# Kernel tuning notes

Measured on AMD Instinct MI355X. Metric: run time of the kernel, lower is better.

The kernel has to match this reference:

```python
import jax, jax.numpy as jnp
import numpy as np

N_NODES = 100000
N_EDGES = 1600000
NFEAT = 128
NHID = 128
NS = 64
NCLASS = 16
B = 8192


def setup_inputs() -> dict:
    key = jax.random.key(0)
    ks = jax.random.split(key, 12)
    s = jax.random.normal(ks[0], (B, NS), dtype=jnp.float32)
    x = jax.random.normal(ks[1], (N_NODES, NFEAT), dtype=jnp.float32)
    row = jax.random.randint(ks[2], (N_EDGES,), 0, N_NODES)
    col = jax.random.randint(ks[3], (N_EDGES,), 0, N_NODES)
    val = jax.random.uniform(ks[4], (N_EDGES,), dtype=jnp.float32)
    index = jax.random.randint(ks[5], (B,), 0, N_NODES)
    # learned parameters (glorot-ish scale)
    W1 = jax.random.normal(ks[6], (NFEAT, NHID), dtype=jnp.float32) / np.sqrt(NFEAT)
    b1 = jnp.zeros((NHID,), dtype=jnp.float32)
    W2 = jax.random.normal(ks[7], (NHID, NHID), dtype=jnp.float32) / np.sqrt(NHID)
    b2 = jnp.zeros((NHID,), dtype=jnp.float32)
    Wl = jax.random.normal(ks[8], (NHID + NS, NCLASS), dtype=jnp.float32) / np.sqrt(NHID + NS)
    bl = jnp.zeros((NCLASS,), dtype=jnp.float32)
    return {"s": s, "x": x, "row": row, "col": col, "val": val,
            "index": index, "W1": W1, "b1": b1, "W2": W2, "b2": b2,
            "Wl": Wl, "bl": bl}


def reference(s, x, row, col, val, index, W1, b1, W2, b2, Wl, bl):
    n = x.shape[0]

    def spmm(h):
        # adj @ h with adj in COO form: out[r] += val_e * h[c]
        return jax.ops.segment_sum(val[:, None] * h[col], row, num_segments=n)

    # dropout is identity in eval mode (training=False)
    h = jax.nn.relu(spmm(x @ W1) + b1)          # gc1 + relu
    h = spmm(h @ W2) + b2                        # gc2
    z = jnp.concatenate([h[index], s], axis=1) @ Wl + bl  # [B, nclass]
    return jax.nn.log_softmax(z, axis=1)
```

## Files before the change

kernel.cpp:

```cpp
#include <hip/hip_runtime.h>
#include <hip/hip_fp16.h>
#include <math.h>

#define N_NODES 100000
#define N_EDGES 1600000
#define NFEAT 128
#define NHID 128
#define NS 64
#define NCLASS 16
#define BB 8192

#define B1_SHIFT 11
#define NB1 49
#define SUB_SHIFT 5
#define NSUB 3125
#define CHUNKA 2048
#define HWG 256
#define BINC_CAP 2048

#define NSLICE 8
#define SLICEF 16

typedef unsigned long long ull;
typedef unsigned int uint;


__device__ __forceinline__ unsigned short f2bf(float f) {
  unsigned int u = __float_as_uint(f);
  return (unsigned short)((u + 0x7fffu + ((u >> 16) & 1u)) >> 16);
}
__device__ __forceinline__ unsigned int packbf2(float lo, float hi) {
  return (unsigned int)f2bf(lo) | ((unsigned int)f2bf(hi) << 16);
}


__device__ __forceinline__ __half2 h2zero() {
  return __builtin_bit_cast(__half2, 0u);
}
__device__ __forceinline__ __half2 h2shfl_add(__half2 a, int m) {
  int t = __shfl_xor(__builtin_bit_cast(int, a), m);
  return __hadd2(a, __builtin_bit_cast(__half2, t));
}
__device__ __forceinline__ uint relu2(uint u) {
  uint mm = ((u >> 15) & 0x10001u) * 0xFFFFu;
  return u & ~mm;
}
union U4H { uint4 u4; __half2 h[4]; };

__device__ __forceinline__ void fma_row_h(__half2* acc, __half2 v, uint4 u) {
  U4H q; q.u4 = u;
#pragma unroll
  for (int k = 0; k < 4; ++k) acc[k] = __hfma2(v, q.h[k], acc[k]);
}
__device__ __forceinline__ __half2 edge_vh2(uint e) {
  uint hb = e >> 17;
  return __builtin_bit_cast(__half2, hb * 0x10001u);
}


__device__ __forceinline__ ull pack_edge(float v, int r, int c) {
  return ((ull)(__float_as_uint(v) >> 2) << 34) | ((ull)(unsigned)r << 17) | (unsigned)c;
}
__device__ __forceinline__ int edge_col(ull p) { return (int)(p & 0x1FFFFu); }
__device__ __forceinline__ int edge_row(ull p) { return (int)((unsigned)(p >> 17) & 0x1FFFFu); }
__device__ __forceinline__ float edge_val(ull p) {
  return __uint_as_float(((unsigned)(p >> 34)) << 2);
}
__device__ __forceinline__ uint pack4(ull p) {
  uint hb = (uint)__half_as_ushort(__float2half(edge_val(p)));
  return (uint)edge_col(p) | (hb << 17);
}
__device__ __forceinline__ int keep_test(const uint* keep, int r) {
  return (keep[r >> 5] >> (r & 31)) & 1u;
}


__global__ __launch_bounds__(256) void selbuild_kernel(const int* __restrict__ index,
                                                       int* __restrict__ sel,
                                                       uint* __restrict__ keep) {
  int t = blockIdx.x * 256 + threadIdx.x;
  int r = index[t];
  sel[r] = 1;
  atomicOr(&keep[r >> 5], 1u << (r & 31));
}

__global__ __launch_bounds__(256) void selflag_kernel(const int* __restrict__ row,
                                                      const int* __restrict__ col,
                                                      const int* __restrict__ sel,
                                                      uint* __restrict__ keep) {
  int i = blockIdx.x * blockDim.x + threadIdx.x;
  int stride = gridDim.x * blockDim.x;
  for (; i < N_EDGES; i += stride)
    if (sel[row[i]]) {
      int c = col[i];
      atomicOr(&keep[c >> 5], 1u << (c & 31));
    }
}


__global__ __launch_bounds__(256) void rdesc_kernel(const uint* __restrict__ keep,
                                                    const int* __restrict__ offs,
                                                    ull* __restrict__ rdesc,
                                                    int* __restrict__ nkept) {
  int w = blockIdx.x * 256 + threadIdx.x;
  if (w >= NSUB) return;
  uint b = keep[w];
  int c = __popc(b);
  if (!c) return;
  int base = atomicAdd(nkept, c);
  int r0 = w << 5;
  while (b) {
    int i = __ffs(b) - 1;
    int r = r0 + i;
    int s0 = offs[r], s1 = offs[r + 1];
    rdesc[base++] = (ull)(uint)r | ((ull)(uint)s0 << 17) | ((ull)(uint)(s1 - s0) << 39);
    b &= b - 1;
  }
}

__global__ __launch_bounds__(256) void sdesc_kernel(const int* __restrict__ index,
                                                    const int* __restrict__ offs,
                                                    ull* __restrict__ sdesc) {
  int b = blockIdx.x * 256 + threadIdx.x;
  int r = index[b];
  int s0 = offs[r];
  sdesc[b] = (ull)(uint)s0 | ((ull)(uint)(offs[r + 1] - s0) << 22);
}


__global__ __launch_bounds__(256) void histsub_kernel(const int* __restrict__ row,
                                                      const uint* __restrict__ keep,
                                                      int* __restrict__ subcnt) {
  __shared__ int lh[NSUB];
  int tid = threadIdx.x;
  for (int i = tid; i < NSUB; i += 256) lh[i] = 0;
  __syncthreads();
  for (long i = (long)blockIdx.x * 256 + tid; i < N_EDGES; i += (long)HWG * 256) {
    int r = row[i];
    if (keep_test(keep, r)) atomicAdd(&lh[r >> SUB_SHIFT], 1);
  }
  __syncthreads();
  for (int i = tid; i < NSUB; i += 256) {
    int c = lh[i];
    if (c) atomicAdd(&subcnt[i], c);
  }
}


__global__ __launch_bounds__(1024) void scanall_kernel(const int* __restrict__ subcnt,
                                                       int* __restrict__ sub_offs,
                                                       int* __restrict__ gcur1,
                                                       int* __restrict__ gcur2) {
  __shared__ int sd[1024];
  int tid = threadIdx.x;
  int b0 = tid * 4;
  int vv[4];
  int loc = 0;
#pragma unroll
  for (int k = 0; k < 4; ++k) {
    int i = b0 + k;
    vv[k] = (i < NSUB) ? subcnt[i] : 0;
    loc += vv[k];
  }
  sd[tid] = loc;
  __syncthreads();
  for (int o = 1; o < 1024; o <<= 1) {
    int add = (tid >= o) ? sd[tid - o] : 0;
    __syncthreads();
    sd[tid] += add;
    __syncthreads();
  }
  int pre = sd[tid] - loc;
#pragma unroll
  for (int k = 0; k < 4; ++k) {
    int i = b0 + k;
    if (i < NSUB) {
      sub_offs[i] = pre;
      gcur2[i] = pre;
      if ((i & 63) == 0) gcur1[i >> 6] = pre;
      pre += vv[k];
    }
  }
  if (tid == 1023) sub_offs[NSUB] = sd[1023];
}


__global__ __launch_bounds__(256) void binA_kernel(const int* __restrict__ row,
                                                   const int* __restrict__ col,
                                                   const float* __restrict__ val,
                                                   const uint* __restrict__ keep,
                                                   int* __restrict__ gcur1,
                                                   ull* __restrict__ ebuf1) {
  __shared__ ull stage[CHUNKA];
  __shared__ short bkt[CHUNKA];
  __shared__ int hist[NB1], lofs[NB1 + 1], lcur[NB1], gbase[NB1];
  int tid = threadIdx.x;
  for (long base = (long)blockIdx.x * CHUNKA; base < N_EDGES; base += (long)gridDim.x * CHUNKA) {
    int cnt = (int)min((long)CHUNKA, (long)N_EDGES - base);
    if (tid < NB1) hist[tid] = 0;
    __syncthreads();
    ull e[8]; int bk[8];
#pragma unroll
    for (int v = 0; v < 8; ++v) {
      int i = v * 256 + tid;
      bk[v] = -1;
      if (i < cnt) {
        long g = base + i;
        int r = row[g];
        if (keep_test(keep, r)) {
          e[v] = pack_edge(val[g], r, col[g]);
          bk[v] = r >> B1_SHIFT;
          atomicAdd(&hist[bk[v]], 1);
        }
      }
    }
    __syncthreads();
    if (tid < 64) {
      int h = (tid < NB1) ? hist[tid] : 0;
      int x = h;
      for (int o = 1; o < 64; o <<= 1) {
        int y = __shfl_up(x, o);
        if (tid >= o) x += y;
      }
      if (tid < NB1) { lofs[tid] = x - h; lcur[tid] = x - h; }
      if (tid == 63) lofs[NB1] = x;
    }
    __syncthreads();
#pragma unroll
    for (int v = 0; v < 8; ++v) {
      if (bk[v] >= 0) {
        int pos = atomicAdd(&lcur[bk[v]], 1);
        stage[pos] = e[v];
        bkt[pos] = (short)bk[v];
      }
    }
    __syncthreads();
    if (tid < NB1) {
      int h = hist[tid];
      if (h > 0) gbase[tid] = atomicAdd(&gcur1[tid], h);
    }
    __syncthreads();
    int tot = lofs[NB1];
    for (int s = tid; s < tot; s += 256) {
      int lo = bkt[s];
      ebuf1[gbase[lo] + (s - lofs[lo])] = stage[s];
    }
    __syncthreads();
  }
}


__global__ __launch_bounds__(256) void binB_kernel(const ull* __restrict__ ebuf1,
                                                   const int* __restrict__ sub_offs,
                                                   int* __restrict__ gcur2,
                                                   ull* __restrict__ edat8) {
  __shared__ ull stage[CHUNKA];
  __shared__ short bkt[CHUNKA];
  __shared__ int hist[64], lofs[65], lcur[64], gbase[64];
  int tid = threadIdx.x;
  int b1 = blockIdx.x >> 3, w = blockIdx.x & 7;
  int rbeg = sub_offs[b1 << 6];
  int rend = sub_offs[min((b1 + 1) << 6, NSUB)];
  for (int base = rbeg + w * CHUNKA; base < rend; base += 8 * CHUNKA) {
    int cnt = min(CHUNKA, rend - base);
    if (tid < 64) hist[tid] = 0;
    __syncthreads();
    ull e[8]; int bk[8];
#pragma unroll
    for (int v = 0; v < 8; ++v) {
      int i = v * 256 + tid;
      bk[v] = -1;
      if (i < cnt) {
        e[v] = ebuf1[base + i];
        bk[v] = (edge_row(e[v]) >> SUB_SHIFT) - (b1 << 6);
        atomicAdd(&hist[bk[v]], 1);
      }
    }
    __syncthreads();
    if (tid < 64) {
      int h = hist[tid];
      int x = h;
      for (int o = 1; o < 64; o <<= 1) {
        int y = __shfl_up(x, o);
        if (tid >= o) x += y;
      }
      lofs[tid] = x - h;
      lcur[tid] = x - h;
      if (tid == 63) lofs[64] = x;
    }
    __syncthreads();
#pragma unroll
    for (int v = 0; v < 8; ++v) {
      if (bk[v] >= 0) {
        int pos = atomicAdd(&lcur[bk[v]], 1);
        stage[pos] = e[v];
        bkt[pos] = (short)bk[v];
      }
    }
    __syncthreads();
    if (tid < 64) {
      int h = hist[tid];
      if (h > 0) gbase[tid] = atomicAdd(&gcur2[(b1 << 6) + tid], h);
    }
    __syncthreads();
    for (int s = tid; s < cnt; s += 256) {
      int lo = bkt[s];
      edat8[gbase[lo] + (s - lofs[lo])] = stage[s];
    }
    __syncthreads();
  }
}


__global__ __launch_bounds__(256) void binC_kernel(const int* __restrict__ sub_offs,
                                                   const ull* __restrict__ edat8,
                                                   ull* __restrict__ ebuf1,
                                                   uint* __restrict__ edat4,
                                                   int* __restrict__ offs) {
  __shared__ ull es[BINC_CAP];
  __shared__ int rcnt[32], rcur[32];
  int s = blockIdx.x, tid = threadIdx.x;
  int r0 = s << SUB_SHIFT;
  int beg = sub_offs[s], end = sub_offs[s + 1];
  int n = end - beg;
  if (tid < 32) rcnt[tid] = 0;
  __syncthreads();
  if (n <= BINC_CAP) {
    for (int i = tid; i < n; i += 256) {
      ull p = edat8[beg + i];
      es[i] = p;
      atomicAdd(&rcnt[edge_row(p) & 31], 1);
    }
    __syncthreads();
    if (tid < 32) {
      int h = rcnt[tid];
      int x = h;
      for (int o = 1; o < 32; o <<= 1) {
        int y = __shfl_up(x, o, 32);
        if (tid >= o) x += y;
      }
      rcur[tid] = x - h;
      offs[r0 + tid] = beg + x - h;
      if (s == NSUB - 1 && tid == 31) offs[N_NODES] = end;
    }
    __syncthreads();
    for (int i = tid; i < n; i += 256) {
      ull p = es[i];
      int pos = atomicAdd(&rcur[edge_row(p) & 31], 1);
      edat4[beg + pos] = pack4(p);
    }
  } else {
    for (int i = tid; i < n; i += 256) {
      ull p = edat8[beg + i];
      ebuf1[beg + i] = p;
      atomicAdd(&rcnt[edge_row(p) & 31], 1);
    }
    __syncthreads();
    if (tid < 32) {
      int h = rcnt[tid];
      int x = h;
      for (int o = 1; o < 32; o <<= 1) {
        int y = __shfl_up(x, o, 32);
        if (tid >= o) x += y;
      }
      rcur[tid] = x - h;
      offs[r0 + tid] = beg + x - h;
      if (s == NSUB - 1 && tid == 31) offs[N_NODES] = end;
    }
    __syncthreads();
    for (int i = tid; i < n; i += 256) {
      ull p = ebuf1[beg + i];
      int pos = atomicAdd(&rcur[edge_row(p) & 31], 1);
      edat4[beg + pos] = pack4(p);
    }
  }
}


typedef __attribute__((ext_vector_type(8))) __bf16 bf16x8;
typedef __attribute__((ext_vector_type(4))) float f32x4;
union FragU { uint4 u; bf16x8 b; };

#define LDSTR 68

__global__ __launch_bounds__(256) void gemm1_kernel(const float* __restrict__ A,
                                                    const float* __restrict__ W,
                                                    unsigned short* __restrict__ C,
                                                    int nrows) {
  __shared__ uint As_s[64 * LDSTR];
  __shared__ uint Wt_s[128 * LDSTR];
  int tid = threadIdx.x;
  int rbase = blockIdx.x * 64;

  {
    int n = tid & 127, hh = tid >> 7;
#pragma unroll
    for (int kk = 0; kk < 32; ++kk) {
      int kc = hh * 32 + kk;
      Wt_s[n * LDSTR + kc] = packbf2(W[(2 * kc) * 128 + n], W[(2 * kc + 1) * 128 + n]);
    }
  }
  {
    const float4* src = (const float4*)(A + (long)rbase * 128);
#pragma unroll
    for (int i = 0; i < 8; ++i) {
      int f = i * 256 + tid;
      int m = f >> 5;
      float4 v = (rbase + m < nrows) ? src[f] : make_float4(0.f, 0.f, 0.f, 0.f);
      int c = (f & 31) * 2;
      As_s[m * LDSTR + c]     = packbf2(v.x, v.y);
      As_s[m * LDSTR + c + 1] = packbf2(v.z, v.w);
    }
  }
  __syncthreads();

  int w = tid >> 6, lane = tid & 63;
  int quad = lane >> 4, lr = lane & 15;
  int n0 = w * 32;

  f32x4 acc[4][2];
#pragma unroll
  for (int mt = 0; mt < 4; ++mt)
#pragma unroll
    for (int nt = 0; nt < 2; ++nt) acc[mt][nt] = (f32x4){0.f, 0.f, 0.f, 0.f};

#pragma unroll
  for (int kk = 0; kk < 4; ++kk) {
    int kc = kk * 16 + quad * 4;
    FragU fb0, fb1;
    fb0.u = *(const uint4*)&Wt_s[(n0 + lr) * LDSTR + kc];
    fb1.u = *(const uint4*)&Wt_s[(n0 + 16 + lr) * LDSTR + kc];
#pragma unroll
    for (int mt = 0; mt < 4; ++mt) {
      FragU fa;
      fa.u = *(const uint4*)&As_s[(mt * 16 + lr) * LDSTR + kc];
      acc[mt][0] = __builtin_amdgcn_mfma_f32_16x16x32_bf16(fa.b, fb0.b, acc[mt][0], 0, 0, 0);
      acc[mt][1] = __builtin_amdgcn_mfma_f32_16x16x32_bf16(fa.b, fb1.b, acc[mt][1], 0, 0, 0);
    }
  }

#pragma unroll
  for (int mt = 0; mt < 4; ++mt) {
#pragma unroll
    for (int nt = 0; nt < 2; ++nt) {
      __half* cs = (__half*)(C + (size_t)(w * 2 + nt) * (N_NODES * SLICEF));
#pragma unroll
      for (int r = 0; r < 4; ++r) {
        int row = rbase + mt * 16 + quad * 4 + r;
        if (row < nrows) cs[(size_t)row * SLICEF + lr] = __float2half(acc[mt][nt][r]);
      }
    }
  }
}


__global__ __launch_bounds__(256) void gemm2f_kernel(const float* __restrict__ g2,
                                                     const float* __restrict__ W2,
                                                     const float* __restrict__ b2,
                                                     const float* __restrict__ s_in,
                                                     const float* __restrict__ Wl,
                                                     const float* __restrict__ bl,
                                                     float* __restrict__ out) {
  __shared__ uint smem[13056];
  uint* Wt_s = smem;
  uint* As_s = smem + 128 * LDSTR;
  float* ts  = (float*)smem;
  float* Wls = (float*)(smem + 128 * LDSTR);
  int tid = threadIdx.x;
  int rbase = blockIdx.x * 64;

  {
    int n = tid & 127, hh = tid >> 7;
#pragma unroll
    for (int kk = 0; kk < 32; ++kk) {
      int kc = hh * 32 + kk;
      Wt_s[n * LDSTR + kc] = packbf2(W2[(2 * kc) * 128 + n], W2[(2 * kc + 1) * 128 + n]);
    }
  }
  {
    const float4* src = (const float4*)(g2 + (long)rbase * 128);
#pragma unroll
    for (int i = 0; i < 8; ++i) {
      int f = i * 256 + tid;
      int m = f >> 5, c = (f & 31) * 2;
      float4 v = src[f];
      As_s[m * LDSTR + c]     = packbf2(v.x, v.y);
      As_s[m * LDSTR + c + 1] = packbf2(v.z, v.w);
    }
  }
  __syncthreads();

  int w = tid >> 6, lane = tid & 63;
  int quad = lane >> 4, lr = lane & 15;
  int n0 = w * 32;

  f32x4 acc[4][2];
#pragma unroll
  for (int mt = 0; mt < 4; ++mt)
#pragma unroll
    for (int nt = 0; nt < 2; ++nt) acc[mt][nt] = (f32x4){0.f, 0.f, 0.f, 0.f};

#pragma unroll
  for (int kk = 0; kk < 4; ++kk) {
    int kc = kk * 16 + quad * 4;
    FragU fb0, fb1;
    fb0.u = *(const uint4*)&Wt_s[(n0 + lr) * LDSTR + kc];
    fb1.u = *(const uint4*)&Wt_s[(n0 + 16 + lr) * LDSTR + kc];
#pragma unroll
    for (int mt = 0; mt < 4; ++mt) {
      FragU fa;
      fa.u = *(const uint4*)&As_s[(mt * 16 + lr) * LDSTR + kc];
      acc[mt][0] = __builtin_amdgcn_mfma_f32_16x16x32_bf16(fa.b, fb0.b, acc[mt][0], 0, 0, 0);
      acc[mt][1] = __builtin_amdgcn_mfma_f32_16x16x32_bf16(fa.b, fb1.b, acc[mt][1], 0, 0, 0);
    }
  }
  __syncthreads();

#pragma unroll
  for (int mt = 0; mt < 4; ++mt) {
#pragma unroll
    for (int nt = 0; nt < 2; ++nt) {
      int col = n0 + nt * 16 + lr;
      float bv = b2[col];
#pragma unroll
      for (int r = 0; r < 4; ++r)
        ts[(mt * 16 + quad * 4 + r) * 129 + col] = acc[mt][nt][r] + bv;
    }
  }
  for (int i = tid; i < 192 * 16; i += 256) Wls[i] = Wl[i];
  __syncthreads();

  int q = lane & 3;
  int mrow = w * 16 + (lane >> 2);
  int b = rbase + mrow;
  float z[16];
#pragma unroll
  for (int c = 0; c < 16; ++c) z[c] = 0.f;
  int k0 = q * 48;
  for (int kk = 0; kk < 48; ++kk) {
    int k = k0 + kk;
    float xv = (k < 128) ? ts[mrow * 129 + k] : s_in[(long)b * 64 + (k - 128)];
    const float* wp = Wls + k * 16;
#pragma unroll
    for (int c = 0; c < 16; ++c) z[c] = fmaf(xv, wp[c], z[c]);
  }
#pragma unroll
  for (int c = 0; c < 16; ++c) {
    z[c] += __shfl_xor(z[c], 1);
    z[c] += __shfl_xor(z[c], 2);
  }
  if (q == 0) {
#pragma unroll
    for (int c = 0; c < 16; ++c) z[c] += bl[c];
    float mx = z[0];
#pragma unroll
    for (int c = 1; c < 16; ++c) mx = fmaxf(mx, z[c]);
    float sum = 0.f;
#pragma unroll
    for (int c = 0; c < 16; ++c) sum += expf(z[c] - mx);
    float lse = mx + logf(sum);
    float4* ob = (float4*)(out + (long)b * 16);
    ob[0] = make_float4(z[0] - lse, z[1] - lse, z[2] - lse, z[3] - lse);
    ob[1] = make_float4(z[4] - lse, z[5] - lse, z[6] - lse, z[7] - lse);
    ob[2] = make_float4(z[8] - lse, z[9] - lse, z[10] - lse, z[11] - lse);
    ob[3] = make_float4(z[12] - lse, z[13] - lse, z[14] - lse, z[15] - lse);
  }
}


__global__ __launch_bounds__(256) void spmm_row_kernel(const ull* __restrict__ rdesc,
                                                       const uint* __restrict__ edat4,
                                                       const unsigned short* __restrict__ a,
                                                       const float* __restrict__ bias,
                                                       unsigned short* __restrict__ h1,
                                                       const int* __restrict__ nkept) {
  int nk = *nkept;
  int rblk = blockIdx.x >> 3;
  if (rblk * 32 >= nk) return;
  int s = blockIdx.x & 7;
  int tid = threadIdx.x, lane = tid & 63;
  int li = rblk * 32 + (tid >> 3);
  int g = (lane >> 1) & 3, h = lane & 1, h8 = h * 8;
  const unsigned short* as = a + (size_t)s * (N_NODES * SLICEF);
  bool active = li < nk;
  int r = 0, j = 0, jend = 0;
  if (active) {
    ull d = rdesc[li];
    r = (int)(d & 0x1FFFFu);
    int start = (int)((d >> 17) & 0x3FFFFFu);
    j = start + g;
    jend = start + (int)(d >> 39);
  }
  __half2 acc[4] = {h2zero(), h2zero(), h2zero(), h2zero()};
  for (; j + 12 < jend; j += 16) {
    uint e0 = edat4[j];
    uint e1 = edat4[j + 4];
    uint e2 = edat4[j + 8];
    uint e3 = edat4[j + 12];
    uint4 u0 = *(const uint4*)(as + (size_t)(e0 & 0x1FFFFu) * SLICEF + h8);
    uint4 u1 = *(const uint4*)(as + (size_t)(e1 & 0x1FFFFu) * SLICEF + h8);
    uint4 u2 = *(const uint4*)(as + (size_t)(e2 & 0x1FFFFu) * SLICEF + h8);
    uint4 u3 = *(const uint4*)(as + (size_t)(e3 & 0x1FFFFu) * SLICEF + h8);
    fma_row_h(acc, edge_vh2(e0), u0);
    fma_row_h(acc, edge_vh2(e1), u1);
    fma_row_h(acc, edge_vh2(e2), u2);
    fma_row_h(acc, edge_vh2(e3), u3);
  }
  if (j + 4 < jend) {
    uint e0 = edat4[j];
    uint e1 = edat4[j + 4];
    uint4 u0 = *(const uint4*)(as + (size_t)(e0 & 0x1FFFFu) * SLICEF + h8);
    uint4 u1 = *(const uint4*)(as + (size_t)(e1 & 0x1FFFFu) * SLICEF + h8);
    fma_row_h(acc, edge_vh2(e0), u0);
    fma_row_h(acc, edge_vh2(e1), u1);
    j += 8;
  }
  if (j < jend) {
    uint e = edat4[j];
    uint4 u = *(const uint4*)(as + (size_t)(e & 0x1FFFFu) * SLICEF + h8);
    fma_row_h(acc, edge_vh2(e), u);
  }
#pragma unroll
  for (int k = 0; k < 4; ++k) {
    acc[k] = h2shfl_add(acc[k], 2);
    acc[k] = h2shfl_add(acc[k], 4);
  }
  if (active && (lane & 6) == 0) {
    const float* bp = bias + s * SLICEF + h8;
    float4 b0 = *(const float4*)bp;
    float4 b1v = *(const float4*)(bp + 4);
    uint4 o;
    o.x = relu2(__builtin_bit_cast(uint, __hadd2(acc[0], __floats2half2_rn(b0.x, b0.y))));
    o.y = relu2(__builtin_bit_cast(uint, __hadd2(acc[1], __floats2half2_rn(b0.z, b0.w))));
    o.z = relu2(__builtin_bit_cast(uint, __hadd2(acc[2], __floats2half2_rn(b1v.x, b1v.y))));
    o.w = relu2(__builtin_bit_cast(uint, __hadd2(acc[3], __floats2half2_rn(b1v.z, b1v.w))));
    *(uint4*)(h1 + (size_t)s * (N_NODES * SLICEF) + (size_t)r * SLICEF + h8) = o;
  }
}

__global__ __launch_bounds__(256) void spmm_sel_kernel(const ull* __restrict__ sdesc,
                                                       const uint* __restrict__ edat4,
                                                       const unsigned short* __restrict__ h1,
                                                       float* __restrict__ g2) {
  int s = blockIdx.x & 7;
  int bblk = blockIdx.x >> 3;
  int tid = threadIdx.x, lane = tid & 63;
  int b = bblk * 32 + (tid >> 3);
  int g = (lane >> 1) & 3, h = lane & 1, h8 = h * 8;
  const unsigned short* hs = h1 + (size_t)s * (N_NODES * SLICEF);
  ull d = sdesc[b];
  int start = (int)(d & 0x3FFFFFu);
  int j = start + g, jend = start + (int)(d >> 22);
  __half2 acc[4] = {h2zero(), h2zero(), h2zero(), h2zero()};
  for (; j + 12 < jend; j += 16) {
    uint e0 = edat4[j];
    uint e1 = edat4[j + 4];
    uint e2 = edat4[j + 8];
    uint e3 = edat4[j + 12];
    uint4 u0 = *(const uint4*)(hs + (size_t)(e0 & 0x1FFFFu) * SLICEF + h8);
    uint4 u1 = *(const uint4*)(hs + (size_t)(e1 & 0x1FFFFu) * SLICEF + h8);
    uint4 u2 = *(const uint4*)(hs + (size_t)(e2 & 0x1FFFFu) * SLICEF + h8);
    uint4 u3 = *(const uint4*)(hs + (size_t)(e3 & 0x1FFFFu) * SLICEF + h8);
    fma_row_h(acc, edge_vh2(e0), u0);
    fma_row_h(acc, edge_vh2(e1), u1);
    fma_row_h(acc, edge_vh2(e2), u2);
    fma_row_h(acc, edge_vh2(e3), u3);
  }
  if (j + 4 < jend) {
    uint e0 = edat4[j];
    uint e1 = edat4[j + 4];
    uint4 u0 = *(const uint4*)(hs + (size_t)(e0 & 0x1FFFFu) * SLICEF + h8);
    uint4 u1 = *(const uint4*)(hs + (size_t)(e1 & 0x1FFFFu) * SLICEF + h8);
    fma_row_h(acc, edge_vh2(e0), u0);
    fma_row_h(acc, edge_vh2(e1), u1);
    j += 8;
  }
  if (j < jend) {
    uint e = edat4[j];
    uint4 u = *(const uint4*)(hs + (size_t)(e & 0x1FFFFu) * SLICEF + h8);
    fma_row_h(acc, edge_vh2(e), u);
  }
#pragma unroll
  for (int k = 0; k < 4; ++k) {
    acc[k] = h2shfl_add(acc[k], 2);
    acc[k] = h2shfl_add(acc[k], 4);
  }
  if ((lane & 6) == 0) {
    float* op = g2 + (size_t)b * 128 + s * SLICEF + h8;
    *(float4*)op = make_float4(__low2float(acc[0]), __high2float(acc[0]),
                               __low2float(acc[1]), __high2float(acc[1]));
    *(float4*)(op + 4) = make_float4(__low2float(acc[2]), __high2float(acc[2]),
                                     __low2float(acc[3]), __high2float(acc[3]));
  }
}


extern "C" void kernel_launch(void* const* d_in, const int* in_sizes, int n_in,
                              void* d_out, int out_size, void* d_ws, size_t ws_size,
                              hipStream_t stream) {
  const float* s_in  = (const float*)d_in[0];
  const float* x     = (const float*)d_in[1];
  const int*   row   = (const int*)d_in[2];
  const int*   col   = (const int*)d_in[3];
  const float* val   = (const float*)d_in[4];
  const int*   index = (const int*)d_in[5];
  const float* W1    = (const float*)d_in[6];
  const float* b1    = (const float*)d_in[7];
  const float* W2    = (const float*)d_in[8];
  const float* b2    = (const float*)d_in[9];
  const float* Wl    = (const float*)d_in[10];
  const float* bl    = (const float*)d_in[11];
  float* out = (float*)d_out;

  ull* edat8 = (ull*)d_ws;
  ull* ebuf1 = edat8 + N_EDGES;
  uint* edat4 = (uint*)ebuf1;
  ull* rdesc = edat8;
  ull* sdesc = edat8 + N_NODES;
  unsigned short* a  = (unsigned short*)(ebuf1 + N_EDGES);
  unsigned short* h1 = a + (size_t)N_NODES * 128;
  float* g2   = (float*)(h1 + (size_t)N_NODES * 128);
  int* sel    = (int*)(g2 + (size_t)BB * 128);
  int* subcnt = sel + N_NODES;
  uint* keep  = (uint*)(subcnt + NSUB);
  int* offs   = (int*)(keep + NSUB);
  int* sub_offs = offs + (N_NODES + 1);
  int* gcur1  = sub_offs + (NSUB + 1);
  int* gcur2  = gcur1 + NB1;
  int* nkept  = gcur2 + NSUB;

  hipMemsetAsync(sel, 0, (N_NODES + 2 * NSUB) * sizeof(int), stream);
  hipMemsetAsync(nkept, 0, sizeof(int), stream);

  selbuild_kernel<<<BB / 256, 256, 0, stream>>>(index, sel, keep);
  selflag_kernel<<<4096, 256, 0, stream>>>(row, col, sel, keep);
  histsub_kernel<<<HWG, 256, 0, stream>>>(row, keep, subcnt);
  scanall_kernel<<<1, 1024, 0, stream>>>(subcnt, sub_offs, gcur1, gcur2);

  binA_kernel<<<512, 256, 0, stream>>>(row, col, val, keep, gcur1, ebuf1);
  binB_kernel<<<NB1 * 8, 256, 0, stream>>>(ebuf1, sub_offs, gcur2, edat8);
  binC_kernel<<<NSUB, 256, 0, stream>>>(sub_offs, edat8, ebuf1, edat4, offs);

  rdesc_kernel<<<(NSUB + 255) / 256, 256, 0, stream>>>(keep, offs, rdesc, nkept);
  sdesc_kernel<<<BB / 256, 256, 0, stream>>>(index, offs, sdesc);

  gemm1_kernel<<<(N_NODES + 63) / 64, 256, 0, stream>>>(x, W1, a, N_NODES);
  spmm_row_kernel<<<NSUB * NSLICE, 256, 0, stream>>>(rdesc, edat4, a, b1, h1, nkept);
  spmm_sel_kernel<<<(BB / 32) * NSLICE, 256, 0, stream>>>(sdesc, edat4, h1, g2);
  gemm2f_kernel<<<BB / 64, 256, 0, stream>>>(g2, W2, b2, s_in, Wl, bl, out);
}
```

Baseline: 317.9 us.

## Replace two-pass LDS-staged binning with direct global-atomic scatter; double gemm1 rows per block

The two-level bucket sort (binA into 49 coarse bins, then binB into 3125 sub-bins) becomes a single kernel in which each kept edge takes its slot with a global atomicAdd on its sub-bucket cursor and writes straight to edat8. This removes one full pass over the edge buffer and the LDS staging, at the cost of heavy global atomic contention and uncoalesced scattered writes. Separately, gemm1 now handles two 64-row tiles per block, so the W1 transpose/convert into LDS is amortised across twice the rows with half as many blocks.

```diff
diff --git a/kernel.cpp b/kernel.cpp
--- a/kernel.cpp
+++ b/kernel.cpp
@@ -10,11 +10,8 @@
 #define NCLASS 16
 #define BB 8192
 
-#define B1_SHIFT 11
-#define NB1 49
 #define SUB_SHIFT 5
 #define NSUB 3125
-#define CHUNKA 2048
 #define HWG 256
 #define BINC_CAP 2048
 
@@ -149,7 +146,6 @@
 
 __global__ __launch_bounds__(1024) void scanall_kernel(const int* __restrict__ subcnt,
                                                        int* __restrict__ sub_offs,
-                                                       int* __restrict__ gcur1,
                                                        int* __restrict__ gcur2) {
   __shared__ int sd[1024];
   int tid = threadIdx.x;
@@ -177,7 +173,6 @@
     if (i < NSUB) {
       sub_offs[i] = pre;
       gcur2[i] = pre;
-      if ((i & 63) == 0) gcur1[i >> 6] = pre;
       pre += vv[k];
     }
   }
@@ -185,129 +180,20 @@
 }
 
 
-__global__ __launch_bounds__(256) void binA_kernel(const int* __restrict__ row,
-                                                   const int* __restrict__ col,
-                                                   const float* __restrict__ val,
-                                                   const uint* __restrict__ keep,
-                                                   int* __restrict__ gcur1,
-                                                   ull* __restrict__ ebuf1) {
-  __shared__ ull stage[CHUNKA];
-  __shared__ short bkt[CHUNKA];
-  __shared__ int hist[NB1], lofs[NB1 + 1], lcur[NB1], gbase[NB1];
-  int tid = threadIdx.x;
-  for (long base = (long)blockIdx.x * CHUNKA; base < N_EDGES; base += (long)gridDim.x * CHUNKA) {
-    int cnt = (int)min((long)CHUNKA, (long)N_EDGES - base);
-    if (tid < NB1) hist[tid] = 0;
-    __syncthreads();
-    ull e[8]; int bk[8];
-#pragma unroll
-    for (int v = 0; v < 8; ++v) {
-      int i = v * 256 + tid;
-      bk[v] = -1;
-      if (i < cnt) {
-        long g = base + i;
-        int r = row[g];
-        if (keep_test(keep, r)) {
-          e[v] = pack_edge(val[g], r, col[g]);
-          bk[v] = r >> B1_SHIFT;
-          atomicAdd(&hist[bk[v]], 1);
-        }
-      }
-    }
-    __syncthreads();
-    if (tid < 64) {
-      int h = (tid < NB1) ? hist[tid] : 0;
-      int x = h;
-      for (int o = 1; o < 64; o <<= 1) {
-        int y = __shfl_up(x, o);
-        if (tid >= o) x += y;
-      }
-      if (tid < NB1) { lofs[tid] = x - h; lcur[tid] = x - h; }
-      if (tid == 63) lofs[NB1] = x;
-    }
-    __syncthreads();
-#pragma unroll
-    for (int v = 0; v < 8; ++v) {
-      if (bk[v] >= 0) {
-        int pos = atomicAdd(&lcur[bk[v]], 1);
-        stage[pos] = e[v];
-        bkt[pos] = (short)bk[v];
-      }
-    }
-    __syncthreads();
-    if (tid < NB1) {
-      int h = hist[tid];
-      if (h > 0) gbase[tid] = atomicAdd(&gcur1[tid], h);
-    }
-    __syncthreads();
-    int tot = lofs[NB1];
-    for (int s = tid; s < tot; s += 256) {
-      int lo = bkt[s];
-      ebuf1[gbase[lo] + (s - lofs[lo])] = stage[s];
-    }
-    __syncthreads();
-  }
-}
-
-
-__global__ __launch_bounds__(256) void binB_kernel(const ull* __restrict__ ebuf1,
-                                                   const int* __restrict__ sub_offs,
-                                                   int* __restrict__ gcur2,
-                                                   ull* __restrict__ edat8) {
-  __shared__ ull stage[CHUNKA];
-  __shared__ short bkt[CHUNKA];
-  __shared__ int hist[64], lofs[65], lcur[64], gbase[64];
-  int tid = threadIdx.x;
-  int b1 = blockIdx.x >> 3, w = blockIdx.x & 7;
-  int rbeg = sub_offs[b1 << 6];
-  int rend = sub_offs[min((b1 + 1) << 6, NSUB)];
-  for (int base = rbeg + w * CHUNKA; base < rend; base += 8 * CHUNKA) {
-    int cnt = min(CHUNKA, rend - base);
-    if (tid < 64) hist[tid] = 0;
-    __syncthreads();
-    ull e[8]; int bk[8];
-#pragma unroll
-    for (int v = 0; v < 8; ++v) {
-      int i = v * 256 + tid;
-      bk[v] = -1;
-      if (i < cnt) {
-        e[v] = ebuf1[base + i];
-        bk[v] = (edge_row(e[v]) >> SUB_SHIFT) - (b1 << 6);
-        atomicAdd(&hist[bk[v]], 1);
-      }
-    }
-    __syncthreads();
-    if (tid < 64) {
-      int h = hist[tid];
-      int x = h;
-      for (int o = 1; o < 64; o <<= 1) {
-        int y = __shfl_up(x, o);
-        if (tid >= o) x += y;
-      }
-      lofs[tid] = x - h;
-      lcur[tid] = x - h;
-      if (tid == 63) lofs[64] = x;
-    }
-    __syncthreads();
-#pragma unroll
-    for (int v = 0; v < 8; ++v) {
-      if (bk[v] >= 0) {
-        int pos = atomicAdd(&lcur[bk[v]], 1);
-        stage[pos] = e[v];
-        bkt[pos] = (short)bk[v];
-      }
-    }
-    __syncthreads();
-    if (tid < 64) {
-      int h = hist[tid];
-      if (h > 0) gbase[tid] = atomicAdd(&gcur2[(b1 << 6) + tid], h);
-    }
-    __syncthreads();
-    for (int s = tid; s < cnt; s += 256) {
-      int lo = bkt[s];
-      edat8[gbase[lo] + (s - lofs[lo])] = stage[s];
-    }
-    __syncthreads();
+__global__ __launch_bounds__(256) void binAB_kernel(const int* __restrict__ row,
+                                                    const int* __restrict__ col,
+                                                    const float* __restrict__ val,
+                                                    const uint* __restrict__ keep,
+                                                    int* __restrict__ gcur2,
+                                                    ull* __restrict__ edat8) {
+  long i = (long)blockIdx.x * 256 + threadIdx.x;
+  long stride = (long)gridDim.x * 256;
+  for (; i < N_EDGES; i += stride) {
+    int r = row[i];
+    if (keep_test(keep, r)) {
+      int pos = atomicAdd(&gcur2[r >> SUB_SHIFT], 1);
+      edat8[pos] = pack_edge(val[i], r, col[i]);
+    }
   }
 }
 
@@ -390,7 +276,6 @@
   __shared__ uint As_s[64 * LDSTR];
   __shared__ uint Wt_s[128 * LDSTR];
   int tid = threadIdx.x;
-  int rbase = blockIdx.x * 64;
 
   {
     int n = tid & 127, hh = tid >> 7;
@@ -400,54 +285,60 @@
       Wt_s[n * LDSTR + kc] = packbf2(W[(2 * kc) * 128 + n], W[(2 * kc + 1) * 128 + n]);
     }
   }
-  {
-    const float4* src = (const float4*)(A + (long)rbase * 128);
-#pragma unroll
-    for (int i = 0; i < 8; ++i) {
-      int f = i * 256 + tid;
-      int m = f >> 5;
-      float4 v = (rbase + m < nrows) ? src[f] : make_float4(0.f, 0.f, 0.f, 0.f);
-      int c = (f & 31) * 2;
-      As_s[m * LDSTR + c]     = packbf2(v.x, v.y);
-      As_s[m * LDSTR + c + 1] = packbf2(v.z, v.w);
-    }
-  }
-  __syncthreads();
 
   int w = tid >> 6, lane = tid & 63;
   int quad = lane >> 4, lr = lane & 15;
   int n0 = w * 32;
 
-  f32x4 acc[4][2];
-#pragma unroll
-  for (int mt = 0; mt < 4; ++mt)
-#pragma unroll
-    for (int nt = 0; nt < 2; ++nt) acc[mt][nt] = (f32x4){0.f, 0.f, 0.f, 0.f};
-
-#pragma unroll
-  for (int kk = 0; kk < 4; ++kk) {
-    int kc = kk * 16 + quad * 4;
-    FragU fb0, fb1;
-    fb0.u = *(const uint4*)&Wt_s[(n0 + lr) * LDSTR + kc];
-    fb1.u = *(const uint4*)&Wt_s[(n0 + 16 + lr) * LDSTR + kc];
+#pragma unroll
+  for (int t = 0; t < 2; ++t) {
+    int rbase = blockIdx.x * 128 + t * 64;
+    __syncthreads();
+    {
+      const float4* src = (const float4*)(A + (long)rbase * 128);
+#pragma unroll
+      for (int i = 0; i < 8; ++i) {
+        int f = i * 256 + tid;
+        int m = f >> 5;
+        float4 v = (rbase + m < nrows) ? src[f] : make_float4(0.f, 0.f, 0.f, 0.f);
+        int c = (f & 31) * 2;
+        As_s[m * LDSTR + c]     = packbf2(v.x, v.y);
+        As_s[m * LDSTR + c + 1] = packbf2(v.z, v.w);
+      }
+    }
+    __syncthreads();
+
+    f32x4 acc[4][2];
+#pragma unroll
+    for (int mt = 0; mt < 4; ++mt)
+#pragma unroll
+      for (int nt = 0; nt < 2; ++nt) acc[mt][nt] = (f32x4){0.f, 0.f, 0.f, 0.f};
+
+#pragma unroll
+    for (int kk = 0; kk < 4; ++kk) {
+      int kc = kk * 16 + quad * 4;
+      FragU fb0, fb1;
+      fb0.u = *(const uint4*)&Wt_s[(n0 + lr) * LDSTR + kc];
+      fb1.u = *(const uint4*)&Wt_s[(n0 + 16 + lr) * LDSTR + kc];
+#pragma unroll
+      for (int mt = 0; mt < 4; ++mt) {
+        FragU fa;
+        fa.u = *(const uint4*)&As_s[(mt * 16 + lr) * LDSTR + kc];
+        acc[mt][0] = __builtin_amdgcn_mfma_f32_16x16x32_bf16(fa.b, fb0.b, acc[mt][0], 0, 0, 0);
+        acc[mt][1] = __builtin_amdgcn_mfma_f32_16x16x32_bf16(fa.b, fb1.b, acc[mt][1], 0, 0, 0);
+      }
+    }
+
 #pragma unroll
     for (int mt = 0; mt < 4; ++mt) {
-      FragU fa;
-      fa.u = *(const uint4*)&As_s[(mt * 16 + lr) * LDSTR + kc];
-      acc[mt][0] = __builtin_amdgcn_mfma_f32_16x16x32_bf16(fa.b, fb0.b, acc[mt][0], 0, 0, 0);
-      acc[mt][1] = __builtin_amdgcn_mfma_f32_16x16x32_bf16(fa.b, fb1.b, acc[mt][1], 0, 0, 0);
-    }
-  }
-
-#pragma unroll
-  for (int mt = 0; mt < 4; ++mt) {
-#pragma unroll
-    for (int nt = 0; nt < 2; ++nt) {
-      __half* cs = (__half*)(C + (size_t)(w * 2 + nt) * (N_NODES * SLICEF));
-#pragma unroll
-      for (int r = 0; r < 4; ++r) {
-        int row = rbase + mt * 16 + quad * 4 + r;
-        if (row < nrows) cs[(size_t)row * SLICEF + lr] = __float2half(acc[mt][nt][r]);
+#pragma unroll
+      for (int nt = 0; nt < 2; ++nt) {
+        __half* cs = (__half*)(C + (size_t)(w * 2 + nt) * (N_NODES * SLICEF));
+#pragma unroll
+        for (int r = 0; r < 4; ++r) {
+          int row = rbase + mt * 16 + quad * 4 + r;
+          if (row < nrows) cs[(size_t)row * SLICEF + lr] = __float2half(acc[mt][nt][r]);
+        }
       }
     }
   }
@@ -725,8 +616,7 @@
   uint* keep  = (uint*)(subcnt + NSUB);
   int* offs   = (int*)(keep + NSUB);
   int* sub_offs = offs + (N_NODES + 1);
-  int* gcur1  = sub_offs + (NSUB + 1);
-  int* gcur2  = gcur1 + NB1;
+  int* gcur2  = sub_offs + (NSUB + 1);
   int* nkept  = gcur2 + NSUB;
 
   hipMemsetAsync(sel, 0, (N_NODES + 2 * NSUB) * sizeof(int), stream);
@@ -735,16 +625,15 @@
   selbuild_kernel<<<BB / 256, 256, 0, stream>>>(index, sel, keep);
   selflag_kernel<<<4096, 256, 0, stream>>>(row, col, sel, keep);
   histsub_kernel<<<HWG, 256, 0, stream>>>(row, keep, subcnt);
-  scanall_kernel<<<1, 1024, 0, stream>>>(subcnt, sub_offs, gcur1, gcur2);
-
-  binA_kernel<<<512, 256, 0, stream>>>(row, col, val, keep, gcur1, ebuf1);
-  binB_kernel<<<NB1 * 8, 256, 0, stream>>>(ebuf1, sub_offs, gcur2, edat8);
+  scanall_kernel<<<1, 1024, 0, stream>>>(subcnt, sub_offs, gcur2);
+
+  binAB_kernel<<<2048, 256, 0, stream>>>(row, col, val, keep, gcur2, edat8);
   binC_kernel<<<NSUB, 256, 0, stream>>>(sub_offs, edat8, ebuf1, edat4, offs);
 
   rdesc_kernel<<<(NSUB + 255) / 256, 256, 0, stream>>>(keep, offs, rdesc, nkept);
   sdesc_kernel<<<BB / 256, 256, 0, stream>>>(index, offs, sdesc);
 
-  gemm1_kernel<<<(N_NODES + 63) / 64, 256, 0, stream>>>(x, W1, a, N_NODES);
+  gemm1_kernel<<<(N_NODES + 127) / 128, 256, 0, stream>>>(x, W1, a, N_NODES);
   spmm_row_kernel<<<NSUB * NSLICE, 256, 0, stream>>>(rdesc, edat4, a, b1, h1, nkept);
   spmm_sel_kernel<<<(BB / 32) * NSLICE, 256, 0, stream>>>(sdesc, edat4, h1, g2);
   gemm2f_kernel<<<BB / 64, 256, 0, stream>>>(g2, W2, b2, s_in, Wl, bl, out);
```

New measurement: 393.7 us. +23.9%, slower.
